# Kernel tuning notes

Hardware: AMD Instinct MI355X
Metric: run time of the kernel (lower is better)

## Reference

```python
import jax, jax.numpy as jnp
import numpy as np

B, H, S, D = 2, 16, 2048, 64
N_SINK = 1


def setup_inputs() -> dict:
    key = jax.random.key(0)
    kq, kk, ks = jax.random.split(key, 3)
    q = jax.random.normal(kq, (B, H, S, D), dtype=jnp.float32)
    k = jax.random.normal(kk, (B, H, S, D), dtype=jnp.float32)
    sinks = jax.random.normal(ks, (B, H, S, N_SINK), dtype=jnp.float32)
    return {"q": q, "k": k, "sinks": sinks}


def reference(q, k, sinks):
    # scores: [B,H,S,S] = q @ k^T
    scores = jnp.einsum("bhqd,bhkd->bhqk", q, k)
    # per-key norm ||k||, broadcast over query dim: [B,H,1,S]
    denom = jnp.sqrt(jnp.sum(k * k, axis=-1))[..., None, :]
    w = scores / denom
    # causal: zero (NOT -inf) above the diagonal, faithful to torch.tril
    w = jnp.tril(w)
    # append learned sink logits: [B,H,S,S+N_SINK]
    w = jnp.concatenate([w, sinks], axis=-1)
    return jax.nn.softmax(w, axis=-1)
```

## Files before the change

kernel.cpp:

```cpp
#include <hip/hip_runtime.h>
#include <hip/hip_fp16.h>
#include <math.h>

#define S 2048
#define D 64
#define BH 32
#define TILE 64
#define NT (S / TILE)
#define SP1 (S + 1)

typedef _Float16 f16;
typedef f16 f16x8 __attribute__((ext_vector_type(8)));
typedef f16 f16x4 __attribute__((ext_vector_type(4)));
typedef float f32x4 __attribute__((ext_vector_type(4)));

#define LDS_PITCH 72

__global__ __launch_bounds__(256) void knorm_kernel(const float* __restrict__ k,
                                                    float* __restrict__ rinv) {
    int row  = (blockIdx.x * 256 + threadIdx.x) >> 6;
    int lane = threadIdx.x & 63;
    float v = k[(size_t)row * D + lane];
    float s = v * v;
    #pragma unroll
    for (int off = 32; off; off >>= 1) s += __shfl_xor(s, off);
    if (lane == 0) rinv[row] = 1.0f / sqrtf(s);
}

__global__ __launch_bounds__(256) void rowsum_kernel(
    const float* __restrict__ q, const float* __restrict__ k,
    const float* __restrict__ sinks, const float* __restrict__ rinv,
    float* __restrict__ inv_l)
{
    __shared__ __align__(16) f16 qs[TILE * LDS_PITCH];
    __shared__ __align__(16) f16 ks[TILE * LDS_PITCH];

    const int it = blockIdx.x;
    const int bh = blockIdx.y;
    const int i0 = it * TILE;
    const int tid  = threadIdx.x;
    const int lane = tid & 63;
    const int w    = tid >> 6;
    const int m    = lane & 15;
    const int quad = lane >> 4;

    const float* qbase = q + (size_t)bh * S * D;
    const float* kbase = k + (size_t)bh * S * D;

    {
        int r  = tid >> 4;
        int c4 = (tid & 15) * 4;
        #pragma unroll
        for (int rb = 0; rb < 4; rb++) {
            int row = rb * 16 + r;
            float4 v = *(const float4*)(qbase + (size_t)(i0 + row) * D + c4);
            f16x4 hv; hv[0] = (f16)v.x; hv[1] = (f16)v.y; hv[2] = (f16)v.z; hv[3] = (f16)v.w;
            *(f16x4*)&qs[row * LDS_PITCH + c4] = hv;
        }
    }
    __syncthreads();

    f16x8 a0 = *(const f16x8*)&qs[(w * 16 + m) * LDS_PITCH + 0  + quad * 8];
    f16x8 a1 = *(const f16x8*)&qs[(w * 16 + m) * LDS_PITCH + 32 + quad * 8];

    float rowsum[4] = {0.f, 0.f, 0.f, 0.f};
    const int ib = i0 + w * 16 + quad * 4;

    for (int jt = 0; jt <= it; jt++) {
        const int j0 = jt * TILE;
        __syncthreads();
        {
            int r  = tid >> 4;
            int c4 = (tid & 15) * 4;
            #pragma unroll
            for (int rb = 0; rb < 4; rb++) {
                int row = rb * 16 + r;
                float4 v = *(const float4*)(kbase + (size_t)(j0 + row) * D + c4);
                f16x4 hv; hv[0] = (f16)v.x; hv[1] = (f16)v.y; hv[2] = (f16)v.z; hv[3] = (f16)v.w;
                *(f16x4*)&ks[row * LDS_PITCH + c4] = hv;
            }
        }
        __syncthreads();

        const bool diag = (jt == it);
        #pragma unroll
        for (int st = 0; st < 4; st++) {
            f16x8 b0 = *(const f16x8*)&ks[(st * 16 + m) * LDS_PITCH + 0  + quad * 8];
            f16x8 b1 = *(const f16x8*)&ks[(st * 16 + m) * LDS_PITCH + 32 + quad * 8];
            f32x4 acc = {0.f, 0.f, 0.f, 0.f};
            acc = __builtin_amdgcn_mfma_f32_16x16x32_f16(a0, b0, acc, 0, 0, 0);
            acc = __builtin_amdgcn_mfma_f32_16x16x32_f16(a1, b1, acc, 0, 0, 0);
            const int j = j0 + st * 16 + m;
            const float rj = rinv[bh * S + j];
            #pragma unroll
            for (int r = 0; r < 4; r++) {
                float e = __expf(acc[r] * rj);
                if (diag && j > ib + r) e = 0.0f;
                rowsum[r] += e;
            }
        }
    }

    #pragma unroll
    for (int off = 1; off < 16; off <<= 1)
        #pragma unroll
        for (int r = 0; r < 4; r++) rowsum[r] += __shfl_xor(rowsum[r], off);

    if (m == 0) {
        #pragma unroll
        for (int r = 0; r < 4; r++) {
            int i = ib + r;
            float l = rowsum[r] + (float)(S - 1 - i) + __expf(sinks[bh * S + i]);
            inv_l[bh * S + i] = 1.0f / l;
        }
    }
}

__global__ __launch_bounds__(256) void out_kernel(
    const float* __restrict__ q, const float* __restrict__ k,
    const float* __restrict__ rinv, const float* __restrict__ inv_l,
    float* __restrict__ out)
{
    const int jt = blockIdx.x;
    const int it = blockIdx.y;
    const int bh = blockIdx.z;
    const int i0 = it * TILE, j0 = jt * TILE;
    const int tid = threadIdx.x;
    float* obase = out + (size_t)bh * S * SP1;

    if (jt > it) {
        const int rb = tid >> 6;
        const int c  = tid & 63;
        #pragma unroll
        for (int r = 0; r < 16; r++) {
            int i = i0 + rb * 16 + r;
            obase[(size_t)i * SP1 + j0 + c] = inv_l[bh * S + i];
        }
        return;
    }

    __shared__ __align__(16) f16 qs[TILE * LDS_PITCH];
    __shared__ __align__(16) f16 ks[TILE * LDS_PITCH];

    const int lane = tid & 63;
    const int w    = tid >> 6;
    const int m    = lane & 15;
    const int quad = lane >> 4;

    const float* qbase = q + (size_t)bh * S * D;
    const float* kbase = k + (size_t)bh * S * D;

    {
        int r  = tid >> 4;
        int c4 = (tid & 15) * 4;
        #pragma unroll
        for (int rb = 0; rb < 4; rb++) {
            int row = rb * 16 + r;
            float4 vq = *(const float4*)(qbase + (size_t)(i0 + row) * D + c4);
            f16x4 hq; hq[0] = (f16)vq.x; hq[1] = (f16)vq.y; hq[2] = (f16)vq.z; hq[3] = (f16)vq.w;
            *(f16x4*)&qs[row * LDS_PITCH + c4] = hq;
            float4 vk = *(const float4*)(kbase + (size_t)(j0 + row) * D + c4);
            f16x4 hk; hk[0] = (f16)vk.x; hk[1] = (f16)vk.y; hk[2] = (f16)vk.z; hk[3] = (f16)vk.w;
            *(f16x4*)&ks[row * LDS_PITCH + c4] = hk;
        }
    }
    __syncthreads();

    f16x8 a0 = *(const f16x8*)&qs[(w * 16 + m) * LDS_PITCH + 0  + quad * 8];
    f16x8 a1 = *(const f16x8*)&qs[(w * 16 + m) * LDS_PITCH + 32 + quad * 8];

    const int ib = i0 + w * 16 + quad * 4;
    float il[4];
    #pragma unroll
    for (int r = 0; r < 4; r++) il[r] = inv_l[bh * S + ib + r];

    const bool diag = (jt == it);
    #pragma unroll
    for (int st = 0; st < 4; st++) {
        f16x8 b0 = *(const f16x8*)&ks[(st * 16 + m) * LDS_PITCH + 0  + quad * 8];
        f16x8 b1 = *(const f16x8*)&ks[(st * 16 + m) * LDS_PITCH + 32 + quad * 8];
        f32x4 acc = {0.f, 0.f, 0.f, 0.f};
        acc = __builtin_amdgcn_mfma_f32_16x16x32_f16(a0, b0, acc, 0, 0, 0);
        acc = __builtin_amdgcn_mfma_f32_16x16x32_f16(a1, b1, acc, 0, 0, 0);
        const int j = j0 + st * 16 + m;
        const float rj = rinv[bh * S + j];
        #pragma unroll
        for (int r = 0; r < 4; r++) {
            float val = __expf(acc[r] * rj) * il[r];
            if (diag && j > ib + r) val = il[r];
            obase[(size_t)(ib + r) * SP1 + j] = val;
        }
    }
}

__global__ __launch_bounds__(256) void sink_kernel(const float* __restrict__ sinks,
                                                   const float* __restrict__ inv_l,
                                                   float* __restrict__ out) {
    int t = blockIdx.x * 256 + threadIdx.x;
    out[(size_t)t * SP1 + S] = __expf(sinks[t]) * inv_l[t];
}

extern "C" void kernel_launch(void* const* d_in, const int* in_sizes, int n_in,
                              void* d_out, int out_size, void* d_ws, size_t ws_size,
                              hipStream_t stream) {
    const float* q     = (const float*)d_in[0];
    const float* k     = (const float*)d_in[1];
    const float* sinks = (const float*)d_in[2];
    float* out = (float*)d_out;

    float* rinv  = (float*)d_ws;
    float* inv_l = rinv + BH * S;

    knorm_kernel<<<dim3(BH * S / 4), 256, 0, stream>>>(k, rinv);
    rowsum_kernel<<<dim3(NT, BH), 256, 0, stream>>>(q, k, sinks, rinv, inv_l);
    out_kernel<<<dim3(NT, NT, BH), 256, 0, stream>>>(q, k, rinv, inv_l, out);
    sink_kernel<<<dim3(BH * S / 256), 256, 0, stream>>>(sinks, inv_l, out);
}
```

Before: 787.3 us.

## Fuse rowsum, output and sink kernels into one per-row-tile kernel with f16 prepass

A prep kernel now converts q to f16 and k to normalized f16 in one pass, which removes the per-key rinv scaling and the repeated fp32-to-f16 conversion. One main kernel per query tile computes the row sums, then recomputes the scores and writes the causal tiles through an LDS staging buffer for coalesced stores. It also writes the constant upper-triangle fill with float4 stores and writes the sink column, replacing the separate out and sink kernels. The risk is less parallelism and load imbalance: there are only NT*BH blocks, and work per block grows with the row index, where the old output grid was NT*NT*BH. K fragments are also read straight from global memory with no LDS sharing.

```diff
diff --git a/kernel.cpp b/kernel.cpp
--- a/kernel.cpp
+++ b/kernel.cpp
@@ -8,196 +8,133 @@
 #define TILE 64
 #define NT (S / TILE)
 #define SP1 (S + 1)
+#define OS_PITCH 66
 
 typedef _Float16 f16;
 typedef f16 f16x8 __attribute__((ext_vector_type(8)));
-typedef f16 f16x4 __attribute__((ext_vector_type(4)));
 typedef float f32x4 __attribute__((ext_vector_type(4)));
 
-#define LDS_PITCH 72
-
-__global__ __launch_bounds__(256) void knorm_kernel(const float* __restrict__ k,
-                                                    float* __restrict__ rinv) {
+__global__ __launch_bounds__(256) void prep_kernel(const float* __restrict__ q,
+                                                   const float* __restrict__ k,
+                                                   f16* __restrict__ qh,
+                                                   f16* __restrict__ kh) {
     int row  = (blockIdx.x * 256 + threadIdx.x) >> 6;
     int lane = threadIdx.x & 63;
-    float v = k[(size_t)row * D + lane];
-    float s = v * v;
+    size_t idx = (size_t)row * D + lane;
+    float kv = k[idx];
+    float s = kv * kv;
     #pragma unroll
     for (int off = 32; off; off >>= 1) s += __shfl_xor(s, off);
-    if (lane == 0) rinv[row] = 1.0f / sqrtf(s);
+    float rinv = rsqrtf(s);
+    kh[idx] = (f16)(kv * rinv);
+    qh[idx] = (f16)q[idx];
 }
 
-__global__ __launch_bounds__(256) void rowsum_kernel(
-    const float* __restrict__ q, const float* __restrict__ k,
-    const float* __restrict__ sinks, const float* __restrict__ rinv,
-    float* __restrict__ inv_l)
-{
-    __shared__ __align__(16) f16 qs[TILE * LDS_PITCH];
-    __shared__ __align__(16) f16 ks[TILE * LDS_PITCH];
+__global__ __launch_bounds__(256) void main_kernel(const f16* __restrict__ qh,
+                                                   const f16* __restrict__ kh,
+                                                   const float* __restrict__ sinks,
+                                                   float* __restrict__ out) {
+    __shared__ __align__(16) float os[TILE * OS_PITCH];
 
-    const int it = blockIdx.x;
-    const int bh = blockIdx.y;
-    const int i0 = it * TILE;
+    const int it   = blockIdx.x;
+    const int bh   = blockIdx.y;
+    const int i0   = it * TILE;
     const int tid  = threadIdx.x;
     const int lane = tid & 63;
     const int w    = tid >> 6;
     const int m    = lane & 15;
     const int quad = lane >> 4;
 
-    const float* qbase = q + (size_t)bh * S * D;
-    const float* kbase = k + (size_t)bh * S * D;
+    const f16* qb = qh + (size_t)bh * S * D;
+    const f16* kb = kh + (size_t)bh * S * D;
+    float* obase  = out + (size_t)bh * S * SP1;
 
-    {
-        int r  = tid >> 4;
-        int c4 = (tid & 15) * 4;
-        #pragma unroll
-        for (int rb = 0; rb < 4; rb++) {
-            int row = rb * 16 + r;
-            float4 v = *(const float4*)(qbase + (size_t)(i0 + row) * D + c4);
-            f16x4 hv; hv[0] = (f16)v.x; hv[1] = (f16)v.y; hv[2] = (f16)v.z; hv[3] = (f16)v.w;
-            *(f16x4*)&qs[row * LDS_PITCH + c4] = hv;
-        }
-    }
-    __syncthreads();
+    const int arow = i0 + w * 16 + m;
+    f16x8 a0 = *(const f16x8*)(qb + (size_t)arow * D + quad * 8);
+    f16x8 a1 = *(const f16x8*)(qb + (size_t)arow * D + 32 + quad * 8);
 
-    f16x8 a0 = *(const f16x8*)&qs[(w * 16 + m) * LDS_PITCH + 0  + quad * 8];
-    f16x8 a1 = *(const f16x8*)&qs[(w * 16 + m) * LDS_PITCH + 32 + quad * 8];
+    const int rbase = w * 16 + quad * 4;
+    const int ib    = i0 + rbase;
 
     float rowsum[4] = {0.f, 0.f, 0.f, 0.f};
-    const int ib = i0 + w * 16 + quad * 4;
-
     for (int jt = 0; jt <= it; jt++) {
         const int j0 = jt * TILE;
-        __syncthreads();
-        {
-            int r  = tid >> 4;
-            int c4 = (tid & 15) * 4;
-            #pragma unroll
-            for (int rb = 0; rb < 4; rb++) {
-                int row = rb * 16 + r;
-                float4 v = *(const float4*)(kbase + (size_t)(j0 + row) * D + c4);
-                f16x4 hv; hv[0] = (f16)v.x; hv[1] = (f16)v.y; hv[2] = (f16)v.z; hv[3] = (f16)v.w;
-                *(f16x4*)&ks[row * LDS_PITCH + c4] = hv;
-            }
-        }
-        __syncthreads();
-
         const bool diag = (jt == it);
         #pragma unroll
         for (int st = 0; st < 4; st++) {
-            f16x8 b0 = *(const f16x8*)&ks[(st * 16 + m) * LDS_PITCH + 0  + quad * 8];
-            f16x8 b1 = *(const f16x8*)&ks[(st * 16 + m) * LDS_PITCH + 32 + quad * 8];
+            const int j = j0 + st * 16 + m;
+            f16x8 b0 = *(const f16x8*)(kb + (size_t)j * D + quad * 8);
+            f16x8 b1 = *(const f16x8*)(kb + (size_t)j * D + 32 + quad * 8);
             f32x4 acc = {0.f, 0.f, 0.f, 0.f};
             acc = __builtin_amdgcn_mfma_f32_16x16x32_f16(a0, b0, acc, 0, 0, 0);
             acc = __builtin_amdgcn_mfma_f32_16x16x32_f16(a1, b1, acc, 0, 0, 0);
-            const int j = j0 + st * 16 + m;
-            const float rj = rinv[bh * S + j];
             #pragma unroll
             for (int r = 0; r < 4; r++) {
-                float e = __expf(acc[r] * rj);
-                if (diag && j > ib + r) e = 0.0f;
+                float e = __expf(acc[r]);
+                if (diag && j > ib + r) e = 0.f;
                 rowsum[r] += e;
             }
         }
     }
-
     #pragma unroll
     for (int off = 1; off < 16; off <<= 1)
         #pragma unroll
         for (int r = 0; r < 4; r++) rowsum[r] += __shfl_xor(rowsum[r], off);
 
-    if (m == 0) {
+    float il[4], se[4];
+    #pragma unroll
+    for (int r = 0; r < 4; r++) {
+        int i = ib + r;
+        se[r] = __expf(sinks[bh * S + i]);
+        il[r] = 1.0f / (rowsum[r] + (float)(S - 1 - i) + se[r]);
+    }
+
+    for (int jt = 0; jt <= it; jt++) {
+        const int j0 = jt * TILE;
+        const bool diag = (jt == it);
         #pragma unroll
-        for (int r = 0; r < 4; r++) {
-            int i = ib + r;
-            float l = rowsum[r] + (float)(S - 1 - i) + __expf(sinks[bh * S + i]);
-            inv_l[bh * S + i] = 1.0f / l;
+        for (int st = 0; st < 4; st++) {
+            const int j = j0 + st * 16 + m;
+            f16x8 b0 = *(const f16x8*)(kb + (size_t)j * D + quad * 8);
+            f16x8 b1 = *(const f16x8*)(kb + (size_t)j * D + 32 + quad * 8);
+            f32x4 acc = {0.f, 0.f, 0.f, 0.f};
+            acc = __builtin_amdgcn_mfma_f32_16x16x32_f16(a0, b0, acc, 0, 0, 0);
+            acc = __builtin_amdgcn_mfma_f32_16x16x32_f16(a1, b1, acc, 0, 0, 0);
+            #pragma unroll
+            for (int r = 0; r < 4; r++) {
+                float v = __expf(acc[r]) * il[r];
+                if (diag && j > ib + r) v = il[r];
+                os[(rbase + r) * OS_PITCH + st * 16 + m] = v;
+            }
+        }
+        #pragma unroll
+        for (int rr = 0; rr < 16; rr++) {
+            int row = w * 16 + rr;
+            obase[(size_t)(i0 + row) * SP1 + j0 + lane] = os[row * OS_PITCH + lane];
         }
     }
-}
 
-__global__ __launch_bounds__(256) void out_kernel(
-    const float* __restrict__ q, const float* __restrict__ k,
-    const float* __restrict__ rinv, const float* __restrict__ inv_l,
-    float* __restrict__ out)
-{
-    const int jt = blockIdx.x;
-    const int it = blockIdx.y;
-    const int bh = blockIdx.z;
-    const int i0 = it * TILE, j0 = jt * TILE;
-    const int tid = threadIdx.x;
-    float* obase = out + (size_t)bh * S * SP1;
-
-    if (jt > it) {
-        const int rb = tid >> 6;
-        const int c  = tid & 63;
-        #pragma unroll
-        for (int r = 0; r < 16; r++) {
-            int i = i0 + rb * 16 + r;
-            obase[(size_t)i * SP1 + j0 + c] = inv_l[bh * S + i];
-        }
-        return;
-    }
-
-    __shared__ __align__(16) f16 qs[TILE * LDS_PITCH];
-    __shared__ __align__(16) f16 ks[TILE * LDS_PITCH];
-
-    const int lane = tid & 63;
-    const int w    = tid >> 6;
-    const int m    = lane & 15;
-    const int quad = lane >> 4;
-
-    const float* qbase = q + (size_t)bh * S * D;
-    const float* kbase = k + (size_t)bh * S * D;
-
-    {
-        int r  = tid >> 4;
-        int c4 = (tid & 15) * 4;
-        #pragma unroll
-        for (int rb = 0; rb < 4; rb++) {
-            int row = rb * 16 + r;
-            float4 vq = *(const float4*)(qbase + (size_t)(i0 + row) * D + c4);
-            f16x4 hq; hq[0] = (f16)vq.x; hq[1] = (f16)vq.y; hq[2] = (f16)vq.z; hq[3] = (f16)vq.w;
-            *(f16x4*)&qs[row * LDS_PITCH + c4] = hq;
-            float4 vk = *(const float4*)(kbase + (size_t)(j0 + row) * D + c4);
-            f16x4 hk; hk[0] = (f16)vk.x; hk[1] = (f16)vk.y; hk[2] = (f16)vk.z; hk[3] = (f16)vk.w;
-            *(f16x4*)&ks[row * LDS_PITCH + c4] = hk;
+    const int jb = (it + 1) * TILE;
+    #pragma unroll
+    for (int rr = 0; rr < 16; rr++) {
+        int row = w * 16 + rr;
+        int i = i0 + row;
+        float v  = __shfl(il[rr & 3], (rr >> 2) * 16);
+        float sv = __shfl(se[rr & 3], (rr >> 2) * 16) * v;
+        float* rowp = obase + (size_t)i * SP1;
+        if (lane == 0) rowp[S] = sv;
+        if (jb < S) {
+            int h = (4 - ((i + jb) & 3)) & 3;
+            if (lane < h) rowp[jb + lane] = v;
+            int start4 = jb + h;
+            int n4 = (S - start4) >> 2;
+            float4 vv = make_float4(v, v, v, v);
+            for (int c = lane; c < n4; c += 64)
+                *(float4*)(rowp + start4 + (size_t)c * 4) = vv;
+            int tail = start4 + (n4 << 2);
+            if (lane < S - tail) rowp[tail + lane] = v;
         }
     }
-    __syncthreads();
-
-    f16x8 a0 = *(const f16x8*)&qs[(w * 16 + m) * LDS_PITCH + 0  + quad * 8];
-    f16x8 a1 = *(const f16x8*)&qs[(w * 16 + m) * LDS_PITCH + 32 + quad * 8];
-
-    const int ib = i0 + w * 16 + quad * 4;
-    float il[4];
-    #pragma unroll
-    for (int r = 0; r < 4; r++) il[r] = inv_l[bh * S + ib + r];
-
-    const bool diag = (jt == it);
-    #pragma unroll
-    for (int st = 0; st < 4; st++) {
-        f16x8 b0 = *(const f16x8*)&ks[(st * 16 + m) * LDS_PITCH + 0  + quad * 8];
-        f16x8 b1 = *(const f16x8*)&ks[(st * 16 + m) * LDS_PITCH + 32 + quad * 8];
-        f32x4 acc = {0.f, 0.f, 0.f, 0.f};
-        acc = __builtin_amdgcn_mfma_f32_16x16x32_f16(a0, b0, acc, 0, 0, 0);
-        acc = __builtin_amdgcn_mfma_f32_16x16x32_f16(a1, b1, acc, 0, 0, 0);
-        const int j = j0 + st * 16 + m;
-        const float rj = rinv[bh * S + j];
-        #pragma unroll
-        for (int r = 0; r < 4; r++) {
-            float val = __expf(acc[r] * rj) * il[r];
-            if (diag && j > ib + r) val = il[r];
-            obase[(size_t)(ib + r) * SP1 + j] = val;
-        }
-    }
-}
-
-__global__ __launch_bounds__(256) void sink_kernel(const float* __restrict__ sinks,
-                                                   const float* __restrict__ inv_l,
-                                                   float* __restrict__ out) {
-    int t = blockIdx.x * 256 + threadIdx.x;
-    out[(size_t)t * SP1 + S] = __expf(sinks[t]) * inv_l[t];
 }
 
 extern "C" void kernel_launch(void* const* d_in, const int* in_sizes, int n_in,
@@ -208,11 +145,9 @@
     const float* sinks = (const float*)d_in[2];
     float* out = (float*)d_out;
 
-    float* rinv  = (float*)d_ws;
-    float* inv_l = rinv + BH * S;
+    f16* qh = (f16*)d_ws;
+    f16* kh = qh + (size_t)BH * S * D;
 
-    knorm_kernel<<<dim3(BH * S / 4), 256, 0, stream>>>(k, rinv);
-    rowsum_kernel<<<dim3(NT, BH), 256, 0, stream>>>(q, k, sinks, rinv, inv_l);
-    out_kernel<<<dim3(NT, NT, BH), 256, 0, stream>>>(q, k, rinv, inv_l, out);
-    sink_kernel<<<dim3(BH * S / 256), 256, 0, stream>>>(sinks, inv_l, out);
+    prep_kernel<<<dim3(BH * S / 4), 256, 0, stream>>>(q, k, qh, kh);
+    main_kernel<<<dim3(NT, BH), 256, 0, stream>>>(qh, kh, sinks, out);
 }
```

Measured after the change: 855.8 us. 1.09x slower.
